# Optimization experiments

Hardware: AMD Instinct MI355X
Metric: run time of the kernel (lower is better)

## Reference

```python
import jax, jax.numpy as jnp
import numpy as np

K = 3        # kernel_size
DIL = 1      # dilation
PAD = 1      # padding (replicate)
RANKS = 3
STAGES = 9
C_OUT = 32


def setup_inputs() -> dict:
    key = jax.random.key(0)
    k1, k2, k3 = jax.random.split(key, 3)
    b, cin, H, W = 2, 3, 160, 160
    x = jax.random.normal(k1, (b, cin, H, W), dtype=jnp.float32)
    head_w = jax.random.normal(k2, (C_OUT, cin), dtype=jnp.float32) * (1.0 / np.sqrt(cin))
    tail_w = jax.random.normal(k3, (cin, C_OUT), dtype=jnp.float32) * (1.0 / np.sqrt(C_OUT))
    alphas = jnp.full((STAGES,), 0.01, dtype=jnp.float32)
    betas = jnp.full((STAGES,), 0.01, dtype=jnp.float32)
    return {"x": x, "head_w": head_w, "tail_w": tail_w, "alphas": alphas, "betas": betas}


def _unfold_like_torch(xp, H, W):
    # xp: [b, C, H+2p, W+2p] replicate-padded. Reproduce torch nn.Unfold output
    # layout [b, C*k*k, H*W] (channel-major, then ki, kj; L row-major over h,w).
    b, C = xp.shape[0], xp.shape[1]
    cols = [xp[:, :, i * DIL:i * DIL + H, j * DIL:j * DIL + W]
            for i in range(K) for j in range(K)]
    patches = jnp.stack(cols, axis=2)            # [b, C, k*k, H, W]
    return patches.reshape(b, C * K * K, H * W)  # torch unfold layout


def reference(x, head_w, tail_w, alphas, betas):
    b, cin, H, W = x.shape
    # head 1x1 conv (no bias) + relu
    xh = jax.nn.relu(jnp.einsum('bchw,oc->bohw', x, head_w))
    xp = jnp.pad(xh, ((0, 0), (0, 0), (PAD, PAD), (PAD, PAD)), mode='edge')
    Xu = _unfold_like_torch(xp, H, W)                 # [b, C*kk, H*W]
    # Faithful to torch: X = unfold.view(b, C, H, W, -1) (row-major reinterpret)
    X = Xu.reshape(b, C_OUT, H, W, K * K)
    U = jnp.repeat(X.mean(axis=-1, keepdims=True), RANKS, axis=-1)  # [b,C,H,W,r]
    V = jnp.repeat(X.mean(axis=1, keepdims=True), RANKS, axis=1)    # [b,r,H,W,kk]
    for i in range(STAGES):
        num_V = jnp.einsum('bchwr,bchwk->brhwk', U, X)
        UV = jnp.einsum('bchwr,brhwk->bchwk', U, V)
        den_V = jnp.einsum('bchwr,bchwk->brhwk', U, UV)
        V = V - betas[i] * (den_V - num_V)
        num_U = jnp.einsum('bchwk,brhwk->bchwr', X, V)
        UV = jnp.einsum('bchwr,brhwk->bchwk', U, V)
        den_U = jnp.einsum('bchwk,brhwk->bchwr', UV, V)
        U = U - alphas[i] * (den_U - num_U)
    center = (K // 2) * K + K // 2
    UVc = jnp.einsum('bchwr,brhwk->bchwk', U, V)[..., center]  # [b,C,H,W]
    out = jax.nn.relu(jnp.einsum('bchw,oc->bohw', UVc, tail_w))
    return out
```

## Files before the change

kernel.cpp:

```cpp
#include <hip/hip_runtime.h>
#include <hip/hip_bf16.h>

#define NB    2
#define HW    25600
#define WDIM  160
#define NSTG  9

template <int CTRL>
__device__ __forceinline__ float dpp_add(float v) {
    int moved = __builtin_amdgcn_update_dpp(0, __float_as_int(v), CTRL, 0xf, 0xf, true);
    return v + __int_as_float(moved);
}

__device__ __forceinline__ float reduce4(float v) {
    v = dpp_add<0xB1>(v);
    v = dpp_add<0x4E>(v);
    return v;
}

__device__ __forceinline__ constexpr int hidx(int i, int j) {
    return (i <= j) ? (9 * i - (i * (i - 1)) / 2 + (j - i))
                    : (9 * j - (j * (j - 1)) / 2 + (i - j));
}

__global__ __launch_bounds__(256, 3) void fused_kernel(const float* __restrict__ x,
                                                       const float* __restrict__ head_w,
                                                       const float* __restrict__ tail_w,
                                                       const float* __restrict__ alphas,
                                                       const float* __restrict__ betas,
                                                       float* __restrict__ out) {
    int sub = threadIdx.x & 3;
    int pid = blockIdx.x * 64 + (threadIdx.x >> 2);
    int b   = blockIdx.x / 400;
    int s2  = pid - b * HW;
    int c0  = sub * 8;

    float al[NSTG], be[NSTG];
#pragma unroll
    for (int i = 0; i < NSTG; ++i) { al[i] = alphas[i]; be[i] = betas[i]; }

    const float* xb0 = x + b * 3 * HW;

    int g9  = s2 * 9;
    int kk0 = g9 / HW;
    int r0  = g9 - kk0 * HW;
    int h0  = r0 / WDIM;
    int w0  = r0 - h0 * WDIM;
    int ki0 = kk0 / 3;
    int dh0 = ki0 - 1,            dw0 = kk0 - ki0 * 3 - 1;
    int kk1 = kk0 + 1;
    int ki1 = kk1 / 3;
    int dh1 = ki1 - 1,            dw1 = kk1 - ki1 * 3 - 1;

    int p[9];
#pragma unroll
    for (int k2 = 0; k2 < 9; ++k2) {
        int r  = r0 + k2;
        int wn = w0 + k2;
        int cw = (wn >= WDIM);
        int w1 = cw ? wn - WDIM : wn;
        int h1 = h0 + cw;
        bool wr = (r >= HW);
        int h  = wr ? 0 : h1;
        int w  = wr ? r - HW : w1;
        int dh = wr ? dh1 : dh0;
        int dw = wr ? dw1 : dw0;
        int hh = min(max(h + dh, 0), 159);
        int ww = min(max(w + dw, 0), 159);
        p[k2]  = hh * WDIM + ww;
    }

    float xv0[9], xv1[9], xv2[9];
#pragma unroll
    for (int k2 = 0; k2 < 9; ++k2) xv0[k2] = xb0[p[k2]];
#pragma unroll
    for (int k2 = 0; k2 < 9; ++k2) xv1[k2] = xb0[HW + p[k2]];
#pragma unroll
    for (int k2 = 0; k2 < 9; ++k2) xv2[k2] = xb0[2 * HW + p[k2]];

    float Hm[45], v0p[9], Gp[3][9];
    {
        float w0h = head_w[c0 * 3 + 0];
        float w1h = head_w[c0 * 3 + 1];
        float w2h = head_w[c0 * 3 + 2];
        float Xc[9];
#pragma unroll
        for (int k = 0; k < 9; ++k)
            Xc[k] = fmaxf(w0h * xv0[k] + w1h * xv1[k] + w2h * xv2[k], 0.f);
#pragma unroll
        for (int i = 0; i < 9; ++i)
#pragma unroll
            for (int jj = i; jj < 9; ++jj)
                Hm[hidx(i, jj)] = Xc[i] * Xc[jj];
#pragma unroll
        for (int k = 0; k < 9; ++k) v0p[k] = Xc[k];
#pragma unroll
        for (int oo = 0; oo < 3; ++oo) {
            float tw = tail_w[oo * 32 + c0];
#pragma unroll
            for (int k = 0; k < 9; ++k) Gp[oo][k] = tw * Xc[k];
        }
    }
#pragma unroll
    for (int j = 1; j < 8; ++j) {
        float w0h = head_w[(c0 + j) * 3 + 0];
        float w1h = head_w[(c0 + j) * 3 + 1];
        float w2h = head_w[(c0 + j) * 3 + 2];
        float Xc[9];
#pragma unroll
        for (int k = 0; k < 9; ++k)
            Xc[k] = fmaxf(w0h * xv0[k] + w1h * xv1[k] + w2h * xv2[k], 0.f);
#pragma unroll
        for (int i = 0; i < 9; ++i)
#pragma unroll
            for (int jj = i; jj < 9; ++jj)
                Hm[hidx(i, jj)] += Xc[i] * Xc[jj];
#pragma unroll
        for (int k = 0; k < 9; ++k) v0p[k] += Xc[k];
#pragma unroll
        for (int oo = 0; oo < 3; ++oo) {
            float tw = tail_w[oo * 32 + c0 + j];
#pragma unroll
            for (int k = 0; k < 9; ++k) Gp[oo][k] += tw * Xc[k];
        }
    }

#pragma unroll
    for (int t = 0; t < 45; ++t) Hm[t] = reduce4(Hm[t]);
    float v[9];
#pragma unroll
    for (int k = 0; k < 9; ++k) v[k] = reduce4(v0p[k]) * (1.f / 32.f);
    float a[9];
#pragma unroll
    for (int k = 0; k < 9; ++k) a[k] = (1.f / 9.f);

#pragma unroll
    for (int i = 0; i < NSTG; ++i) {
        float beta  = be[i];
        float alpha = al[i];
        float b3 = 3.f * beta;
        float a3 = 3.f * alpha;
        float c[9];
#pragma unroll
        for (int r = 0; r < 9; ++r) {
            float t0 = Hm[hidx(r, 0)] * a[0] + Hm[hidx(r, 1)] * a[1];
            float t1 = Hm[hidx(r, 2)] * a[2] + Hm[hidx(r, 3)] * a[3];
            float t2 = Hm[hidx(r, 4)] * a[4] + Hm[hidx(r, 5)] * a[5];
            float t3 = Hm[hidx(r, 6)] * a[6] + Hm[hidx(r, 7)] * a[7];
            c[r] = ((t0 + t1) + (t2 + t3)) + Hm[hidx(r, 8)] * a[8];
        }
        float S = (((a[0] * c[0] + a[1] * c[1]) + (a[2] * c[2] + a[3] * c[3]))
                +  ((a[4] * c[4] + a[5] * c[5]) + (a[6] * c[6] + a[7] * c[7])))
                +  a[8] * c[8];
        float vs = 1.f - b3 * S;
#pragma unroll
        for (int k = 0; k < 9; ++k)
            v[k] = v[k] * vs + beta * c[k];
        float T = (((v[0] * v[0] + v[1] * v[1]) + (v[2] * v[2] + v[3] * v[3]))
                +  ((v[4] * v[4] + v[5] * v[5]) + (v[6] * v[6] + v[7] * v[7])))
                +  v[8] * v[8];
        float us = 1.f - a3 * T;
#pragma unroll
        for (int k = 0; k < 9; ++k)
            a[k] = a[k] * us + alpha * v[k];
    }

    float v4 = v[4];
    float o[3];
#pragma unroll
    for (int oo = 0; oo < 3; ++oo) {
        float t0 = Gp[oo][0] * a[0] + Gp[oo][1] * a[1];
        float t1 = Gp[oo][2] * a[2] + Gp[oo][3] * a[3];
        float t2 = Gp[oo][4] * a[4] + Gp[oo][5] * a[5];
        float t3 = Gp[oo][6] * a[6] + Gp[oo][7] * a[7];
        float d  = ((t0 + t1) + (t2 + t3)) + Gp[oo][8] * a[8];
        float r  = reduce4(d);
        o[oo] = fmaxf(3.f * v4 * r, 0.f);
    }
    if (sub == 0) {
        float* op = out + b * 3 * HW + s2;
        op[0]      = o[0];
        op[HW]     = o[1];
        op[2 * HW] = o[2];
    }
}

extern "C" void kernel_launch(void* const* d_in, const int* in_sizes, int n_in,
                              void* d_out, int out_size, void* d_ws, size_t ws_size,
                              hipStream_t stream) {
    const float* x      = (const float*)d_in[0];
    const float* head_w = (const float*)d_in[1];
    const float* tail_w = (const float*)d_in[2];
    const float* alphas = (const float*)d_in[3];
    const float* betas  = (const float*)d_in[4];
    float*       out    = (float*)d_out;

    fused_kernel<<<dim3(NB * HW * 4 / 256), dim3(256), 0, stream>>>(
        x, head_w, tail_w, alphas, betas, out);
}
```

Measured before the change: 80.52 us.

## Use transpose-reduce via DPP and LDS so each lane runs the iteration for one pixel

```diff
diff --git a/kernel.cpp b/kernel.cpp
--- a/kernel.cpp
+++ b/kernel.cpp
@@ -1,5 +1,4 @@
 #include <hip/hip_runtime.h>
-#include <hip/hip_bf16.h>
 
 #define NB    2
 #define HW    25600
@@ -7,15 +6,8 @@
 #define NSTG  9
 
 template <int CTRL>
-__device__ __forceinline__ float dpp_add(float v) {
-    int moved = __builtin_amdgcn_update_dpp(0, __float_as_int(v), CTRL, 0xf, 0xf, true);
-    return v + __int_as_float(moved);
-}
-
-__device__ __forceinline__ float reduce4(float v) {
-    v = dpp_add<0xB1>(v);
-    v = dpp_add<0x4E>(v);
-    return v;
+__device__ __forceinline__ float dpp_mov(float v) {
+    return __int_as_float(__builtin_amdgcn_update_dpp(0, __float_as_int(v), CTRL, 0xf, 0xf, true));
 }
 
 __device__ __forceinline__ constexpr int hidx(int i, int j) {
@@ -23,113 +15,151 @@
                     : (9 * j - (j * (j - 1)) / 2 + (i - j));
 }
 
-__global__ __launch_bounds__(256, 3) void fused_kernel(const float* __restrict__ x,
-                                                       const float* __restrict__ head_w,
-                                                       const float* __restrict__ tail_w,
-                                                       const float* __restrict__ alphas,
-                                                       const float* __restrict__ betas,
-                                                       float* __restrict__ out) {
-    int sub = threadIdx.x & 3;
-    int pid = blockIdx.x * 64 + (threadIdx.x >> 2);
-    int b   = blockIdx.x / 400;
-    int s2  = pid - b * HW;
-    int c0  = sub * 8;
+__global__ __launch_bounds__(64) void fused_kernel(const float* __restrict__ x,
+                                                   const float* __restrict__ head_w,
+                                                   const float* __restrict__ tail_w,
+                                                   const float* __restrict__ alphas,
+                                                   const float* __restrict__ betas,
+                                                   float* __restrict__ out) {
+    const int lane = threadIdx.x;
+    const int sub  = lane & 3;
+    const int c0   = sub * 8;
+    const bool m1  = (lane & 1) != 0;
+    const bool m2  = (lane & 2) != 0;
+
+    __shared__ float lds[64 * 85];
 
     float al[NSTG], be[NSTG];
 #pragma unroll
     for (int i = 0; i < NSTG; ++i) { al[i] = alphas[i]; be[i] = betas[i]; }
 
-    const float* xb0 = x + b * 3 * HW;
-
-    int g9  = s2 * 9;
-    int kk0 = g9 / HW;
-    int r0  = g9 - kk0 * HW;
-    int h0  = r0 / WDIM;
-    int w0  = r0 - h0 * WDIM;
-    int ki0 = kk0 / 3;
-    int dh0 = ki0 - 1,            dw0 = kk0 - ki0 * 3 - 1;
-    int kk1 = kk0 + 1;
-    int ki1 = kk1 / 3;
-    int dh1 = ki1 - 1,            dw1 = kk1 - ki1 * 3 - 1;
-
-    int p[9];
-#pragma unroll
-    for (int k2 = 0; k2 < 9; ++k2) {
-        int r  = r0 + k2;
-        int wn = w0 + k2;
-        int cw = (wn >= WDIM);
-        int w1 = cw ? wn - WDIM : wn;
-        int h1 = h0 + cw;
-        bool wr = (r >= HW);
-        int h  = wr ? 0 : h1;
-        int w  = wr ? r - HW : w1;
-        int dh = wr ? dh1 : dh0;
-        int dw = wr ? dw1 : dw0;
-        int hh = min(max(h + dh, 0), 159);
-        int ww = min(max(w + dw, 0), 159);
-        p[k2]  = hh * WDIM + ww;
+    float hw[8][3];
+#pragma unroll
+    for (int j = 0; j < 8; ++j)
+#pragma unroll
+        for (int ci = 0; ci < 3; ++ci) hw[j][ci] = head_w[(c0 + j) * 3 + ci];
+    float tw[3][8];
+#pragma unroll
+    for (int oo = 0; oo < 3; ++oo)
+#pragma unroll
+        for (int j = 0; j < 8; ++j) tw[oo][j] = tail_w[oo * 32 + c0 + j];
+
+    const int bimg    = blockIdx.x / 400;
+    const int base_s2 = blockIdx.x * 64 - bimg * HW;
+    const float* xb0  = x + bimg * 3 * HW;
+
+#pragma unroll 1
+    for (int bb = 0; bb < 4; ++bb) {
+        const int s2 = base_s2 + bb * 16 + (lane >> 2);
+
+        int g9  = s2 * 9;
+        int kk0 = g9 / HW;
+        int r0  = g9 - kk0 * HW;
+        int h0  = r0 / WDIM;
+        int w0  = r0 - h0 * WDIM;
+        int ki0 = kk0 / 3;
+        int dh0 = ki0 - 1,            dw0 = kk0 - ki0 * 3 - 1;
+        int kk1 = kk0 + 1;
+        int ki1 = kk1 / 3;
+        int dh1 = ki1 - 1,            dw1 = kk1 - ki1 * 3 - 1;
+
+        int p[9];
+#pragma unroll
+        for (int k2 = 0; k2 < 9; ++k2) {
+            int r  = r0 + k2;
+            int wn = w0 + k2;
+            int cw = (wn >= WDIM);
+            int w1 = cw ? wn - WDIM : wn;
+            int h1 = h0 + cw;
+            bool wr = (r >= HW);
+            int h  = wr ? 0 : h1;
+            int w  = wr ? r - HW : w1;
+            int dh = wr ? dh1 : dh0;
+            int dw = wr ? dw1 : dw0;
+            int hh = min(max(h + dh, 0), 159);
+            int ww = min(max(w + dw, 0), 159);
+            p[k2]  = hh * WDIM + ww;
+        }
+
+        float xv0[9], xv1[9], xv2[9];
+#pragma unroll
+        for (int k2 = 0; k2 < 9; ++k2) xv0[k2] = xb0[p[k2]];
+#pragma unroll
+        for (int k2 = 0; k2 < 9; ++k2) xv1[k2] = xb0[HW + p[k2]];
+#pragma unroll
+        for (int k2 = 0; k2 < 9; ++k2) xv2[k2] = xb0[2 * HW + p[k2]];
+
+        float Hp[45], v0p[9], Gpp[27];
+        {
+            float Xc[9];
+#pragma unroll
+            for (int k = 0; k < 9; ++k)
+                Xc[k] = fmaxf(hw[0][0] * xv0[k] + hw[0][1] * xv1[k] + hw[0][2] * xv2[k], 0.f);
+#pragma unroll
+            for (int i = 0; i < 9; ++i)
+#pragma unroll
+                for (int jj = i; jj < 9; ++jj)
+                    Hp[hidx(i, jj)] = Xc[i] * Xc[jj];
+#pragma unroll
+            for (int k = 0; k < 9; ++k) v0p[k] = Xc[k];
+#pragma unroll
+            for (int oo = 0; oo < 3; ++oo)
+#pragma unroll
+                for (int k = 0; k < 9; ++k) Gpp[oo * 9 + k] = tw[oo][0] * Xc[k];
+        }
+#pragma unroll
+        for (int j = 1; j < 8; ++j) {
+            float Xc[9];
+#pragma unroll
+            for (int k = 0; k < 9; ++k)
+                Xc[k] = fmaxf(hw[j][0] * xv0[k] + hw[j][1] * xv1[k] + hw[j][2] * xv2[k], 0.f);
+#pragma unroll
+            for (int i = 0; i < 9; ++i)
+#pragma unroll
+                for (int jj = i; jj < 9; ++jj)
+                    Hp[hidx(i, jj)] += Xc[i] * Xc[jj];
+#pragma unroll
+            for (int k = 0; k < 9; ++k) v0p[k] += Xc[k];
+#pragma unroll
+            for (int oo = 0; oo < 3; ++oo)
+#pragma unroll
+                for (int k = 0; k < 9; ++k) Gpp[oo * 9 + k] += tw[oo][j] * Xc[k];
+        }
+
+        auto getP = [&](int e) -> float {
+            if (e < 45) return Hp[e];
+            if (e < 54) return v0p[e - 45];
+            if (e < 81) return Gpp[e - 54];
+            return 0.f;
+        };
+
+        const int slotbase = (bb * 16 + (lane >> 2)) * 85;
+#pragma unroll
+        for (int g = 0; g < 21; ++g) {
+            float P0 = getP(4 * g + 0), P1 = getP(4 * g + 1);
+            float P2 = getP(4 * g + 2), P3 = getP(4 * g + 3);
+            float a0 = m2 ? P2 : P0;
+            float s0 = m2 ? P0 : P2;
+            a0 += dpp_mov<0x4E>(s0);
+            float a1 = m2 ? P3 : P1;
+            float s1 = m2 ? P1 : P3;
+            a1 += dpp_mov<0x4E>(s1);
+            float fin = m1 ? a1 : a0;
+            float sB  = m1 ? a0 : a1;
+            fin += dpp_mov<0xB1>(sB);
+            lds[slotbase + 4 * g + sub] = fin;
+        }
     }
 
-    float xv0[9], xv1[9], xv2[9];
-#pragma unroll
-    for (int k2 = 0; k2 < 9; ++k2) xv0[k2] = xb0[p[k2]];
-#pragma unroll
-    for (int k2 = 0; k2 < 9; ++k2) xv1[k2] = xb0[HW + p[k2]];
-#pragma unroll
-    for (int k2 = 0; k2 < 9; ++k2) xv2[k2] = xb0[2 * HW + p[k2]];
-
-    float Hm[45], v0p[9], Gp[3][9];
-    {
-        float w0h = head_w[c0 * 3 + 0];
-        float w1h = head_w[c0 * 3 + 1];
-        float w2h = head_w[c0 * 3 + 2];
-        float Xc[9];
-#pragma unroll
-        for (int k = 0; k < 9; ++k)
-            Xc[k] = fmaxf(w0h * xv0[k] + w1h * xv1[k] + w2h * xv2[k], 0.f);
-#pragma unroll
-        for (int i = 0; i < 9; ++i)
-#pragma unroll
-            for (int jj = i; jj < 9; ++jj)
-                Hm[hidx(i, jj)] = Xc[i] * Xc[jj];
-#pragma unroll
-        for (int k = 0; k < 9; ++k) v0p[k] = Xc[k];
-#pragma unroll
-        for (int oo = 0; oo < 3; ++oo) {
-            float tw = tail_w[oo * 32 + c0];
-#pragma unroll
-            for (int k = 0; k < 9; ++k) Gp[oo][k] = tw * Xc[k];
-        }
-    }
-#pragma unroll
-    for (int j = 1; j < 8; ++j) {
-        float w0h = head_w[(c0 + j) * 3 + 0];
-        float w1h = head_w[(c0 + j) * 3 + 1];
-        float w2h = head_w[(c0 + j) * 3 + 2];
-        float Xc[9];
-#pragma unroll
-        for (int k = 0; k < 9; ++k)
-            Xc[k] = fmaxf(w0h * xv0[k] + w1h * xv1[k] + w2h * xv2[k], 0.f);
-#pragma unroll
-        for (int i = 0; i < 9; ++i)
-#pragma unroll
-            for (int jj = i; jj < 9; ++jj)
-                Hm[hidx(i, jj)] += Xc[i] * Xc[jj];
-#pragma unroll
-        for (int k = 0; k < 9; ++k) v0p[k] += Xc[k];
-#pragma unroll
-        for (int oo = 0; oo < 3; ++oo) {
-            float tw = tail_w[oo * 32 + c0 + j];
-#pragma unroll
-            for (int k = 0; k < 9; ++k) Gp[oo][k] += tw * Xc[k];
-        }
-    }
-
-#pragma unroll
-    for (int t = 0; t < 45; ++t) Hm[t] = reduce4(Hm[t]);
+    __syncthreads();
+
+    const int my = lane * 85;
+    float Hm[45];
+#pragma unroll
+    for (int e = 0; e < 45; ++e) Hm[e] = lds[my + e];
     float v[9];
 #pragma unroll
-    for (int k = 0; k < 9; ++k) v[k] = reduce4(v0p[k]) * (1.f / 32.f);
+    for (int k = 0; k < 9; ++k) v[k] = lds[my + 45 + k] * (1.f / 32.f);
     float a[9];
 #pragma unroll
     for (int k = 0; k < 9; ++k) a[k] = (1.f / 9.f);
@@ -166,22 +196,16 @@
     }
 
     float v4 = v[4];
-    float o[3];
+    float* op = out + bimg * 3 * HW + (base_s2 + lane);
 #pragma unroll
     for (int oo = 0; oo < 3; ++oo) {
-        float t0 = Gp[oo][0] * a[0] + Gp[oo][1] * a[1];
-        float t1 = Gp[oo][2] * a[2] + Gp[oo][3] * a[3];
-        float t2 = Gp[oo][4] * a[4] + Gp[oo][5] * a[5];
-        float t3 = Gp[oo][6] * a[6] + Gp[oo][7] * a[7];
-        float d  = ((t0 + t1) + (t2 + t3)) + Gp[oo][8] * a[8];
-        float r  = reduce4(d);
-        o[oo] = fmaxf(3.f * v4 * r, 0.f);
-    }
-    if (sub == 0) {
-        float* op = out + b * 3 * HW + s2;
-        op[0]      = o[0];
-        op[HW]     = o[1];
-        op[2 * HW] = o[2];
+        const int gb = my + 54 + oo * 9;
+        float t0 = lds[gb + 0] * a[0] + lds[gb + 1] * a[1];
+        float t1 = lds[gb + 2] * a[2] + lds[gb + 3] * a[3];
+        float t2 = lds[gb + 4] * a[4] + lds[gb + 5] * a[5];
+        float t3 = lds[gb + 6] * a[6] + lds[gb + 7] * a[7];
+        float d  = ((t0 + t1) + (t2 + t3)) + lds[gb + 8] * a[8];
+        op[oo * HW] = fmaxf(3.f * v4 * d, 0.f);
     }
 }
 
@@ -195,6 +219,6 @@
     const float* betas  = (const float*)d_in[4];
     float*       out    = (float*)d_out;
 
-    fused_kernel<<<dim3(NB * HW * 4 / 256), dim3(256), 0, stream>>>(
+    fused_kernel<<<dim3(NB * HW / 64), dim3(64), 0, stream>>>(
         x, head_w, tail_w, alphas, betas, out);
 }
```

Result: faster. 76.30 us (-5.2%).
